# Kernel tuning notes

Measured on AMD Instinct MI355X. Metric: run time of the kernel, lower is better.

Reference implementation:

```python
import jax, jax.numpy as jnp
import numpy as np

T, WQ, WS, C, H, W = 2, 75, 25, 640, 10, 10
WAY, SHOT = 5, 5
HID = C // 16
SCALE_VALUE = 30.0
ATTEN_SCALE_VALUE = 50.0
FROM_VALUE = 0.5
VALUE_INTERVAL = 0.3
BN_EPS = 1e-5
NORM_EPS = 1e-12


def _leaky(x):
    return jnp.where(x >= 0, x, 0.2 * x)


def _l2norm(x, axis):
    n = jnp.sqrt(jnp.sum(x * x, axis=axis, keepdims=True))
    return x / jnp.maximum(n, NORM_EPS)


def _embed(x, W_conv, bn_gamma, bn_beta, bn_mean, bn_var):
    # 1x1 conv (no bias) + eval-mode BatchNorm + LeakyReLU(0.2)
    # x: [t, n, c, h, w] -> [t, n, c, h, w]
    y = jnp.einsum('oc,tnchw->tnohw', W_conv, x)
    inv = bn_gamma / jnp.sqrt(bn_var + BN_EPS)
    y = y * inv[:, None, None] + (bn_beta - bn_mean * inv)[:, None, None]
    return _leaky(y)


def setup_inputs() -> dict:
    key = jax.random.key(0)
    ks = jax.random.split(key, 5)
    return {
        'query_feat': jax.random.normal(ks[0], (T, WQ, C, H, W), dtype=jnp.float32),
        'support_feat': jax.random.normal(ks[1], (T, WS, C, H, W), dtype=jnp.float32),
        'W_conv': jax.random.normal(ks[2], (C, C), dtype=jnp.float32) * 0.02,
        'bn_gamma': jnp.ones((C,), jnp.float32),
        'bn_beta': jnp.zeros((C,), jnp.float32),
        'bn_mean': jnp.zeros((C,), jnp.float32),
        'bn_var': jnp.ones((C,), jnp.float32),
        'psi_w1': jax.random.normal(ks[3], (C, HID), dtype=jnp.float32) * 0.04,
        'psi_b1': jnp.zeros((HID,), jnp.float32),
        'psi_w2': jax.random.normal(ks[4], (HID, 1), dtype=jnp.float32) * 0.15,
        'psi_b2': jnp.zeros((1,), jnp.float32),
        'way_num': WAY,
        'shot_num': SHOT,
    }


def reference(query_feat, support_feat, W_conv, bn_gamma, bn_beta, bn_mean, bn_var,
              psi_w1, psi_b1, psi_w2, psi_b2, way_num, shot_num):
    t, wq, c, h, w = query_feat.shape
    ws = support_feat.shape[1]
    hw = h * w

    # embedded + normalized features for the gated branch
    w_query = _embed(query_feat, W_conv, bn_gamma, bn_beta, bn_mean, bn_var)
    w_query = w_query.reshape(t, wq, c, hw).transpose(0, 1, 3, 2)      # [t, wq, hw, c]
    w_support = _embed(support_feat, W_conv, bn_gamma, bn_beta, bn_mean, bn_var)
    w_support = w_support.reshape(t, ws, c, hw).transpose(0, 2, 1, 3).reshape(t, c, ws * hw)
    w_query = _l2norm(w_query, axis=3)
    w_support = _l2norm(w_support, axis=1)

    # cosine similarity of embedded features: [t, wq, hw, ws*hw]
    f_x = jnp.einsum('tqpc,tck->tqpk', w_query, w_support)

    # AEAModule: per-location adaptive threshold from f_psi MLP
    hid = _leaky(w_query @ psi_w1 + psi_b1)                            # [t, wq, hw, HID]
    clamp_value = jax.nn.sigmoid(hid @ psi_w2 + psi_b2) * VALUE_INTERVAL + FROM_VALUE
    clamp_fx = jax.nn.sigmoid(ATTEN_SCALE_VALUE * (f_x - clamp_value))
    atten_score = clamp_fx / jnp.maximum(
        jnp.sum(jnp.abs(clamp_fx), axis=-1, keepdims=True), NORM_EPS)  # L1 normalize

    # raw-feature cosine similarity
    qf = _l2norm(query_feat.reshape(t, wq, c, hw).transpose(0, 1, 3, 2), axis=3)
    sf = _l2norm(support_feat.reshape(t, ws, c, hw).transpose(0, 2, 1, 3).reshape(t, c, ws * hw), axis=1)
    match_score = jnp.einsum('tqpc,tck->tqpk', qf, sf)                 # [t, wq, hw, ws*hw]

    # gate, regroup support axis into (way, shot, hw_s), reduce
    ams = (atten_score * match_score).reshape(t, wq, hw, way_num, shot_num, hw)
    score = ams.sum(axis=-1).mean(axis=(2, 4)) * SCALE_VALUE           # [t, wq, way]
    return score
```

## Files before the change

### kernel.cpp

```cpp
#include <hip/hip_runtime.h>
#include <stdint.h>

#define T_    2
#define WQ_   75
#define WS_   25
#define C_    640
#define HW_   100
#define HID_  40
#define WAY_  5
#define QP_   (WQ_*HW_)
#define SP_   (WS_*HW_)
#define QPAD_ 128
#define KPAD_ 512
#define KROWS_ (WAY_*KPAD_)
#define C8_   (C_/8)
#define BM_   256
#define QSTR_ (C8_*QPAD_*8)

typedef _Float16 f16;
typedef _Float16 f16x8 __attribute__((ext_vector_type(8)));
typedef _Float16 f16x4 __attribute__((ext_vector_type(4)));
typedef _Float16 f16x16 __attribute__((ext_vector_type(16)));
typedef float    f32x4 __attribute__((ext_vector_type(4)));
typedef float    f32x16 __attribute__((ext_vector_type(16)));
typedef uint32_t u32;

__device__ __forceinline__ void gl_lds16(const f16* g, f16* l) {
  __builtin_amdgcn_global_load_lds(
      (const __attribute__((address_space(1))) u32*)g,
      (__attribute__((address_space(3))) u32*)l, 16, 0, 0);
}

__global__ __launch_bounds__(512) void k0_invnorm(
    const float* __restrict__ q, const float* __restrict__ s,
    float* __restrict__ rq_inv, float* __restrict__ rq_nrm,
    float* __restrict__ rs_inv, float* __restrict__ rs_nrm) {
  __shared__ float part[4][128];
  int b = blockIdx.x;
  int t = b / (WQ_ + WS_);
  int n = b % (WQ_ + WS_);
  int tid = threadIdx.x;
  int seg = tid >> 7, p = tid & 127;
  const float* base; float* oi; float* on; int idx;
  if (n < WQ_) {
    base = q + ((size_t)(t*WQ_ + n))*C_*HW_;
    idx = t*QP_ + n*HW_ + p; oi = rq_inv; on = rq_nrm;
  } else {
    int m = n - WQ_;
    base = s + ((size_t)(t*WS_ + m))*C_*HW_;
    idx = t*SP_ + m*HW_ + p; oi = rs_inv; on = rs_nrm;
  }
  float ss = 0.f;
  if (p < HW_) {
    for (int c = seg*160; c < seg*160 + 160; ++c) {
      float v = base[c*HW_ + p]; ss += v*v;
    }
  }
  part[seg][p] = ss;
  __syncthreads();
  if (seg == 0 && p < HW_) {
    float tot = part[0][p] + part[1][p] + part[2][p] + part[3][p];
    float nrm = fmaxf(sqrtf(tot), 1e-12f);
    oi[idx] = 1.f/nrm; on[idx] = nrm;
  }
}

__global__ __launch_bounds__(256) void kw_packW(
    const float* __restrict__ W, const float* __restrict__ w1,
    f16* __restrict__ Wr, f16* __restrict__ Wt8, f16* __restrict__ w1t) {
  int idx = blockIdx.x*256 + threadIdx.x;
  if (idx < C_*C8_) {
    int o = idx / C8_, c8 = idx % C8_;
    f16x8 v;
#pragma unroll
    for (int i = 0; i < 8; ++i) v[i] = (f16)W[(size_t)o*C_ + c8*8 + i];
    *reinterpret_cast<f16x8*>(Wr + (size_t)o*C_ + c8*8) = v;
    *reinterpret_cast<f16x8*>(Wt8 + ((size_t)c8*C_ + o)*8) = v;
  } else if (idx < C_*C8_ + 48*C8_) {
    int k2 = idx - C_*C8_;
    int h = k2 / C8_, c8 = k2 % C8_;
    f16x8 v;
#pragma unroll
    for (int i = 0; i < 8; ++i)
      v[i] = (h < HID_) ? (f16)w1[(size_t)(c8*8+i)*HID_ + h] : (f16)0.f;
    *reinterpret_cast<f16x8*>(w1t + (size_t)h*C_ + c8*8) = v;
  }
}

__global__ __launch_bounds__(256) void k1_pack_qraw(
    const float* __restrict__ q, const float* __restrict__ rq_inv,
    f16* __restrict__ Bq_raw) {
  int b = blockIdx.x;
  int ct = b % 10; b /= 10;
  int qq = b % WQ_; int t = b / WQ_;
  int c0 = ct*64;
  size_t tq = (size_t)t*WQ_ + qq;
  __shared__ float lds[64*HW_];
  const float4* s4 = reinterpret_cast<const float4*>(
      q + ((tq)*C_ + c0)*HW_);
  float4* l4 = reinterpret_cast<float4*>(lds);
  for (int i = threadIdx.x; i < 64*HW_/4; i += 256) l4[i] = s4[i];
  __syncthreads();
  for (int ch = threadIdx.x; ch < 8*QPAD_; ch += 256) {
    int lc8 = ch / QPAD_, p = ch % QPAD_;
    float inv = (p < HW_) ? rq_inv[t*QP_ + qq*HW_ + p] : 0.f;
    f16x8 v;
#pragma unroll
    for (int i = 0; i < 8; ++i) {
      float x = (p < HW_) ? lds[(lc8*8 + i)*HW_ + p] : 0.f;
      v[i] = (f16)(x * inv);
    }
    *reinterpret_cast<f16x8*>(Bq_raw + (tq*C8_ + c0/8 + lc8)*((size_t)QPAD_*8) + (size_t)p*8) = v;
  }
}

__global__ __launch_bounds__(256) void k2_pack_sraw(
    const float* __restrict__ s, const float* __restrict__ rs_inv,
    f16* __restrict__ As_raw) {
  int b = blockIdx.x;
  int ct = b % 10; b /= 10;
  int n = b % WS_; int t = b / WS_;
  int c0 = ct*64;
  __shared__ float lds[64*HW_];
  const float4* s4 = reinterpret_cast<const float4*>(
      s + (((size_t)(t*WS_ + n))*C_ + c0)*HW_);
  float4* l4 = reinterpret_cast<float4*>(lds);
  for (int i = threadIdx.x; i < 64*HW_/4; i += 256) l4[i] = s4[i];
  __syncthreads();
  for (int ch = threadIdx.x; ch < HW_*8; ch += 256) {
    int p = ch / 8, cc = ch % 8;
    float inv = rs_inv[t*SP_ + n*HW_ + p];
    f16x8 v;
#pragma unroll
    for (int i = 0; i < 8; ++i) v[i] = (f16)(lds[(cc*8 + i)*HW_ + p] * inv);
    int k = n*HW_ + p;
    int way = k / 500, ki = k % 500;
    size_t row = (size_t)way*KPAD_ + ki;
    *reinterpret_cast<f16x8*>(As_raw + ((size_t)(t*C8_ + c0/8 + cc)*KROWS_ + row)*8) = v;
  }
}

__global__ __launch_bounds__(512) void k3_embed_support(
    const f16* __restrict__ As_raw, const f16* __restrict__ Wt8,
    const float* __restrict__ rs_nrm,
    const float* __restrict__ g, const float* __restrict__ be,
    const float* __restrict__ mu, const float* __restrict__ va,
    f16* __restrict__ As_emb) {
  int b = blockIdx.x;
  int t = b / (KROWS_/64);
  int row0 = (b % (KROWS_/64)) * 64;
  int tid = threadIdx.x, wv = tid >> 6, lane = tid & 63;
  int mf = wv & 3, nh = wv >> 2;
  __shared__ f16 Alds[64*32];
  __shared__ f16 Blds[32*C_];
  __shared__ float rowss[64];
  f32x4 acc[20];
#pragma unroll
  for (int i = 0; i < 20; ++i) acc[i] = (f32x4){0.f,0.f,0.f,0.f};

  for (int cs = 0; cs < 20; ++cs) {
    if (tid < 256) {
      int c8l = tid >> 6, r = tid & 63;
      *reinterpret_cast<f16x8*>(Alds + (c8l*64 + r)*8) =
        *reinterpret_cast<const f16x8*>(
            As_raw + ((size_t)(t*C8_ + cs*4 + c8l)*KROWS_ + row0 + r)*8);
    }
    const f16x8* bsrc = reinterpret_cast<const f16x8*>(Wt8 + (size_t)(cs*4)*C_*8);
    f16x8* bdst = reinterpret_cast<f16x8*>(Blds);
    for (int i = tid; i < 4*C_; i += 512) bdst[i] = bsrc[i];
    __syncthreads();
    f16x8 a = *reinterpret_cast<const f16x8*>(
        Alds + ((lane>>4)*64 + mf*16 + (lane&15))*8);
#pragma unroll
    for (int nf = 0; nf < 20; ++nf) {
      int o = nh*320 + nf*16 + (lane & 15);
      f16x8 bf = *reinterpret_cast<const f16x8*>(Blds + (((lane>>4)*C_) + o)*8);
      acc[nf] = __builtin_amdgcn_mfma_f32_16x16x32_f16(a, bf, acc[nf], 0, 0, 0);
    }
    __syncthreads();
  }

  if (tid < 64) rowss[tid] = 0.f;
  __syncthreads();
  int rg = lane >> 4, cl = lane & 15;
  int prow = row0 + mf*16 + rg*4;
#pragma unroll
  for (int j = 0; j < 4; ++j) {
    int pr = prow + j;
    int way = pr / KPAD_, ki = pr - way*KPAD_;
    bool valid = ki < 500;
    float nrm = valid ? rs_nrm[t*SP_ + way*500 + ki] : 0.f;
    float ssum = 0.f;
#pragma unroll
    for (int nf = 0; nf < 20; ++nf) {
      int o = nh*320 + nf*16 + cl;
      float inv = g[o] / sqrtf(va[o] + 1e-5f);
      float sh = be[o] - mu[o]*inv;
      float y = acc[nf][j]*nrm*inv + sh;
      y = (y >= 0.f) ? y : 0.2f*y;
      if (!valid) y = 0.f;
      acc[nf][j] = y;
      ssum += y*y;
    }
#pragma unroll
    for (int m = 1; m < 16; m <<= 1) ssum += __shfl_xor(ssum, m);
    if (cl == 0) atomicAdd(&rowss[mf*16 + rg*4 + j], ssum);
  }
  __syncthreads();
#pragma unroll
  for (int j = 0; j < 4; ++j) {
    int pr = prow + j;
    int ki = pr - (pr / KPAD_)*KPAD_;
    if (ki >= 500) continue;
    float invn = 1.f / fmaxf(sqrtf(rowss[mf*16 + rg*4 + j]), 1e-12f);
#pragma unroll
    for (int nf = 0; nf < 20; ++nf) {
      int o = nh*320 + nf*16 + cl;
      As_emb[((size_t)(t*C8_ + (o>>3))*KROWS_ + pr)*8 + (o&7)] = (f16)(acc[nf][j]*invn);
    }
  }
}

__global__ __launch_bounds__(256, 3) void k4_embed_query(
    const f16* __restrict__ Wr, const f16* __restrict__ Bq_raw,
    const float* __restrict__ rq_nrm,
    const float* __restrict__ g, const float* __restrict__ be,
    const float* __restrict__ mu, const float* __restrict__ va,
    f16* __restrict__ Bq_emb) {
  __shared__ f16 Ab[3][128*32];
  __shared__ f16 Bb[3][4*QPAD_*8];
  int b = blockIdx.x;
  int ot = b % 5; b /= 5;
  int qq = b % WQ_; int t = b / WQ_;
  int o0 = ot*128;
  size_t tq = (size_t)t*WQ_ + qq;
  int tid = threadIdx.x, w = tid >> 6, lane = tid & 63;
  int la_r = lane >> 2, la_c = lane & 3;

  auto stage = [&](int buf, int cs) {
#pragma unroll
    for (int i = 0; i < 2; ++i) {
      int ca = w*2 + i;
      int r = ca*16 + la_r;
      int sc = la_c ^ (r & 3);
      gl_lds16(Wr + (size_t)(o0 + r)*C_ + cs*32 + sc*8, &Ab[buf][ca*512]);
    }
#pragma unroll
    for (int i = 0; i < 2; ++i) {
      int cb = w*2 + i;
      int c8l = cb >> 1;
      size_t src = (tq*C8_ + cs*4 + c8l)*(size_t)(QPAD_*8) + (size_t)((cb&1)*64 + lane)*8;
      gl_lds16(Bq_raw + src, &Bb[buf][(c8l*QPAD_ + (cb&1)*64)*8]);
    }
  };

  f32x4 acc[2][8];
#pragma unroll
  for (int a = 0; a < 2; ++a)
#pragma unroll
    for (int n = 0; n < 8; ++n) acc[a][n] = (f32x4){0.f,0.f,0.f,0.f};

  stage(0, 0);
  stage(1, 1);
  for (int cs = 0; cs < 20; ++cs) {
    int buf = cs % 3;
    if (cs < 19) asm volatile("s_waitcnt vmcnt(4)" ::: "memory");
    else         asm volatile("s_waitcnt vmcnt(0)" ::: "memory");
    __builtin_amdgcn_s_barrier();
    if (cs < 18) stage((cs+2)%3, cs+2);
    __builtin_amdgcn_s_setprio(1);
    f16x8 fa[2];
#pragma unroll
    for (int mi = 0; mi < 2; ++mi) {
      int R = w*32 + mi*16 + (lane & 15);
      int sc = (lane >> 4) ^ (R & 3);
      fa[mi] = *reinterpret_cast<const f16x8*>(&Ab[buf][R*32 + sc*8]);
    }
#pragma unroll
    for (int nf = 0; nf < 8; ++nf) {
      f16x8 fb = *reinterpret_cast<const f16x8*>(
          &Bb[buf][((lane>>4)*QPAD_ + nf*16 + (lane&15))*8]);
#pragma unroll
      for (int mi = 0; mi < 2; ++mi)
        acc[mi][nf] = __builtin_amdgcn_mfma_f32_16x16x32_f16(fa[mi], fb, acc[mi][nf], 0, 0, 0);
    }
    __builtin_amdgcn_s_setprio(0);
  }

#pragma unroll
  for (int mi = 0; mi < 2; ++mi) {
    int obase = o0 + w*32 + mi*16 + (lane>>4)*4;
    float inv4[4], sh4[4];
#pragma unroll
    for (int j = 0; j < 4; ++j) {
      int o = obase + j;
      inv4[j] = g[o] / sqrtf(va[o] + 1e-5f);
      sh4[j] = be[o] - mu[o]*inv4[j];
    }
#pragma unroll
    for (int nf = 0; nf < 8; ++nf) {
      int pp = nf*16 + (lane & 15);
      float nrmv = (pp < HW_) ? rq_nrm[t*QP_ + qq*HW_ + pp] : 0.f;
      f16x4 vv;
#pragma unroll
      for (int j = 0; j < 4; ++j) {
        float y = (pp < HW_) ? (acc[mi][nf][j]*nrmv*inv4[j] + sh4[j]) : 0.f;
        y = (y >= 0.f) ? y : 0.2f*y;
        vv[j] = (f16)y;
      }
      *reinterpret_cast<f16x4*>(
          &Bq_emb[(tq*C8_ + (obase>>3))*((size_t)QPAD_*8) + (size_t)pp*8 + (obase&7)]) = vv;
    }
  }
}

__global__ __launch_bounds__(256) void k5_colnorm_psi(
    const f16* __restrict__ Bq_emb, const f16* __restrict__ w1t,
    const float* __restrict__ b1, const float* __restrict__ w2,
    const float* __restrict__ b2, float* __restrict__ cv,
    float* __restrict__ invq) {
  __shared__ float ssA[2][QPAD_];
  __shared__ float invs[QPAD_];
  __shared__ float hidL[48*QPAD_];
  int bq = blockIdx.x;
  int tid = threadIdx.x, w = tid >> 6, lane = tid & 63;
  size_t base = (size_t)bq * QSTR_;

  {
    int h2 = tid >> 7, pp = tid & 127;
    float ss = 0.f;
    for (int c8 = h2*40; c8 < h2*40 + 40; ++c8) {
      f16x8 v = *reinterpret_cast<const f16x8*>(&Bq_emb[base + ((size_t)c8*QPAD_ + pp)*8]);
#pragma unroll
      for (int i = 0; i < 8; ++i) { float x = (float)v[i]; ss += x*x; }
    }
    ssA[h2][pp] = ss;
  }
  for (int i = tid; i < 48*QPAD_; i += 256) hidL[i] = 0.f;
  __syncthreads();
  if (tid < QPAD_) {
    float ss = ssA[0][tid] + ssA[1][tid];
    float inv = (ss > 0.f) ? (1.f / fmaxf(sqrtf(ss), 1e-12f)) : 0.f;
    invs[tid] = inv;
    invq[bq*QPAD_ + tid] = inv;
  }

  f32x4 acc[3][8];
#pragma unroll
  for (int a = 0; a < 3; ++a)
#pragma unroll
    for (int n = 0; n < 8; ++n) acc[a][n] = (f32x4){0.f,0.f,0.f,0.f};
  for (int r = 0; r < 5; ++r) {
    int cs = w + r*4;
    f16x8 fa[3];
#pragma unroll
    for (int mf = 0; mf < 3; ++mf) {
      int R = mf*16 + (lane & 15);
      fa[mf] = *reinterpret_cast<const f16x8*>(&w1t[(size_t)R*C_ + cs*32 + (lane>>4)*8]);
    }
#pragma unroll
    for (int nf = 0; nf < 8; ++nf) {
      f16x8 fb = *reinterpret_cast<const f16x8*>(
          &Bq_emb[base + ((size_t)(cs*4 + (lane>>4))*QPAD_ + nf*16 + (lane&15))*8]);
#pragma unroll
      for (int mf = 0; mf < 3; ++mf)
        acc[mf][nf] = __builtin_amdgcn_mfma_f32_16x16x32_f16(fa[mf], fb, acc[mf][nf], 0, 0, 0);
    }
  }
  __syncthreads();
  for (int rr = 0; rr < 4; ++rr) {
    if (w == rr) {
#pragma unroll
      for (int mf = 0; mf < 3; ++mf)
#pragma unroll
        for (int nf = 0; nf < 8; ++nf)
#pragma unroll
          for (int j = 0; j < 4; ++j) {
            int row = mf*16 + (lane>>4)*4 + j;
            int col = nf*16 + (lane & 15);
            hidL[row*QPAD_ + col] += acc[mf][nf][j];
          }
    }
    __syncthreads();
  }
  if (tid < QPAD_) {
    float inv = invs[tid];
    float z = b2[0];
    for (int h = 0; h < HID_; ++h) {
      float hv = hidL[h*QPAD_ + tid]*inv + b1[h];
      hv = (hv >= 0.f) ? hv : 0.2f*hv;
      z += hv*w2[h];
    }
    cv[bq*QPAD_ + tid] = 0.3f/(1.f + __expf(-z)) + 0.5f;
  }
}

__global__ __launch_bounds__(256, 2) void k6_main(
    const f16* __restrict__ As_emb, const f16* __restrict__ As_raw,
    const f16* __restrict__ Bq_emb, const f16* __restrict__ Bq_raw,
    const float* __restrict__ cv, const float* __restrict__ invq,
    float* __restrict__ Spart, float* __restrict__ L1part) {
  __shared__ f16 Ab[3][4*BM_*8];
  __shared__ f16 Bb[3][4*QPAD_*8];
  __shared__ float cvs[QPAD_], iqs[QPAD_], Ss[QPAD_], L1s[QPAD_];

  int bid = blockIdx.x;
  int xcd = bid & 7, j0 = bid >> 3;
  int l = (xcd < 4) ? xcd*188 + j0 : 752 + (xcd-4)*187 + j0;
  int kt = l & 1; int m = l >> 1;
  int q = m % WQ_; int gidx = m / WQ_;
  int t = gidx / WAY_, way = gidx - t*WAY_;

  int tid = threadIdx.x, w = tid >> 6, lane = tid & 63;
  size_t tq = (size_t)t*WQ_ + q;
  if (tid < QPAD_) {
    cvs[tid] = cv[tq*QPAD_ + tid];
    iqs[tid] = invq[tq*QPAD_ + tid];
    Ss[tid] = 0.f; L1s[tid] = 0.f;
  }
  int wrow0 = w*64;
  size_t rowb = (size_t)way*KPAD_ + (size_t)kt*BM_;

  const size_t aoff = ((size_t)(t*C8_ + w)*KROWS_ + rowb + lane)*8;
  const size_t boff = ((tq*C8_ + w)*(size_t)QPAD_ + lane)*8;
  const f16* pA = As_raw + aoff;
  const f16* pB = Bq_raw + boff;
  const f16* pA1 = As_emb + aoff;
  const f16* pB1 = Bq_emb + boff;
  const int CS_A = 4*KROWS_*8;
  const int CS_B = 4*QPAD_*8;

  auto stage = [&](int buf, const f16* a, const f16* bsrc) {
    f16* da = &Ab[buf][(size_t)w*BM_*8];
    f16* db = &Bb[buf][(size_t)w*QPAD_*8];
    gl_lds16(a,        da);
    gl_lds16(a + 512,  da + 512);
    gl_lds16(a + 1024, da + 1024);
    gl_lds16(a + 1536, da + 1536);
    gl_lds16(bsrc,       db);
    gl_lds16(bsrc + 512, db + 512);
  };

  f32x16 acc[2][4];
  f16x16 mtc[2][4];
#pragma unroll
  for (int mi = 0; mi < 2; ++mi)
#pragma unroll
    for (int nf = 0; nf < 4; ++nf) acc[mi][nf] = (f32x16)(0.f);
  float Sl[4] = {0,0,0,0}, L1l[4] = {0,0,0,0};

  stage(0, pA, pB); pA += CS_A; pB += CS_B;
  stage(1, pA, pB); pA += CS_A; pB += CS_B;

  for (int ph = 0; ph < 40; ++ph) {
    if (ph == 18) { pA = pA1; pB = pB1; }
    int buf = ph % 3;
    if (ph < 39) asm volatile("s_waitcnt vmcnt(6)" ::: "memory");
    else         asm volatile("s_waitcnt vmcnt(0)" ::: "memory");
    __builtin_amdgcn_s_barrier();
    if (ph < 38) { stage((ph+2)%3, pA, pB); pA += CS_A; pB += CS_B; }
    __builtin_amdgcn_s_setprio(1);
    const f16* Abuf = Ab[buf];
    const f16* Bbuf = Bb[buf];
    int r0 = wrow0 + (lane & 31);
#pragma unroll
    for (int ks = 0; ks < 2; ++ks) {
      int c8l = ks*2 + (lane >> 5);
      f16x8 fa0 = *reinterpret_cast<const f16x8*>(&Abuf[(c8l*BM_ + r0)*8]);
      f16x8 fa1 = *reinterpret_cast<const f16x8*>(&Abuf[(c8l*BM_ + r0 + 32)*8]);
#pragma unroll
      for (int nf = 0; nf < 4; ++nf) {
        f16x8 fb = *reinterpret_cast<const f16x8*>(
            &Bbuf[(c8l*QPAD_ + nf*32 + (lane & 31))*8]);
        acc[0][nf] = __builtin_amdgcn_mfma_f32_32x32x16_f16(fa0, fb, acc[0][nf], 0, 0, 0);
        acc[1][nf] = __builtin_amdgcn_mfma_f32_32x32x16_f16(fa1, fb, acc[1][nf], 0, 0, 0);
      }
    }
    __builtin_amdgcn_s_setprio(0);

    if (ph == 19) {
#pragma unroll
      for (int mi = 0; mi < 2; ++mi)
#pragma unroll
        for (int nf = 0; nf < 4; ++nf) {
#pragma unroll
          for (int jj = 0; jj < 16; ++jj) {
            mtc[mi][nf][jj] = (f16)fminf(fmaxf(acc[mi][nf][jj], -8.f), 8.f);
            acc[mi][nf][jj] = 0.f;
          }
        }
    } else if (ph == 39) {
#pragma unroll
      for (int nf = 0; nf < 4; ++nf) {
        int col = nf*32 + (lane & 31);
        float cvv = cvs[col];
        float iq = iqs[col];
#pragma unroll
        for (int mi = 0; mi < 2; ++mi)
#pragma unroll
          for (int jj = 0; jj < 16; ++jj) {
            float fx = acc[mi][nf][jj] * iq;
            float sg = 1.f/(1.f + __expf(-50.f*(fx - cvv)));
            Sl[nf]  += sg * (float)mtc[mi][nf][jj];
            L1l[nf] += sg;
          }
      }
    }
  }

#pragma unroll
  for (int nf = 0; nf < 4; ++nf) {
    float vs = Sl[nf] + __shfl_xor(Sl[nf], 32);
    float vl = L1l[nf] + __shfl_xor(L1l[nf], 32);
    if (lane < 32) {
      atomicAdd(&Ss[nf*32 + lane], vs);
      atomicAdd(&L1s[nf*32 + lane], vl);
    }
  }
  __syncthreads();
  if (tid < QPAD_) {
    size_t o = ((tq*WAY_ + way)*2 + kt)*(size_t)QPAD_ + tid;
    Spart[o] = Ss[tid]; L1part[o] = L1s[tid];
  }
}

__global__ __launch_bounds__(128) void k7_reduce(
    const float* __restrict__ Spart, const float* __restrict__ L1part,
    float* __restrict__ out) {
  int b = blockIdx.x;
  int tid = threadIdx.x;
  __shared__ float red[128];
  float contrib[WAY_] = {0,0,0,0,0};
  if (tid < HW_) {
    size_t base = (size_t)b*WAY_*2*QPAD_;
    float l1 = 0.f;
#pragma unroll
    for (int w = 0; w < WAY_; ++w)
#pragma unroll
      for (int k = 0; k < 2; ++k) l1 += L1part[base + (w*2+k)*QPAD_ + tid];
    l1 = fmaxf(l1, 1e-12f);
#pragma unroll
    for (int w = 0; w < WAY_; ++w)
      contrib[w] = (Spart[base + (w*2+0)*QPAD_ + tid] +
                    Spart[base + (w*2+1)*QPAD_ + tid]) / l1;
  }
#pragma unroll
  for (int w = 0; w < WAY_; ++w) {
    red[tid] = contrib[w];
    __syncthreads();
    for (int off = 64; off > 0; off >>= 1) {
      if (tid < off) red[tid] += red[tid + off];
      __syncthreads();
    }
    if (tid == 0) out[b*WAY_ + w] = red[0] * 30.f / (float)(HW_*5);
    __syncthreads();
  }
}

extern "C" void kernel_launch(void* const* d_in, const int* in_sizes, int n_in,
                              void* d_out, int out_size, void* d_ws, size_t ws_size,
                              hipStream_t stream) {
  (void)in_sizes; (void)n_in; (void)out_size; (void)ws_size;
  const float* q  = (const float*)d_in[0];
  const float* s  = (const float*)d_in[1];
  const float* W  = (const float*)d_in[2];
  const float* g  = (const float*)d_in[3];
  const float* be = (const float*)d_in[4];
  const float* mu = (const float*)d_in[5];
  const float* va = (const float*)d_in[6];
  const float* w1 = (const float*)d_in[7];
  const float* b1 = (const float*)d_in[8];
  const float* w2 = (const float*)d_in[9];
  const float* b2 = (const float*)d_in[10];
  float* out = (float*)d_out;
  char* ws = (char*)d_ws;

  size_t off = 0;
  auto nxt = [&](size_t bytes) { size_t o = off; off += (bytes + 255) & ~(size_t)255; return o; };
  float* rq_inv = (float*)(ws + nxt((size_t)T_*QP_*4));
  float* rq_nrm = (float*)(ws + nxt((size_t)T_*QP_*4));
  float* rs_inv = (float*)(ws + nxt((size_t)T_*SP_*4));
  float* rs_nrm = (float*)(ws + nxt((size_t)T_*SP_*4));
  f16* Wr     = (f16*)(ws + nxt((size_t)C_*C_*2));
  f16* Wt8    = (f16*)(ws + nxt((size_t)C_*C_*2));
  f16* w1t    = (f16*)(ws + nxt((size_t)48*C_*2));
  f16* As_raw = (f16*)(ws + nxt((size_t)T_*KROWS_*C_*2));
  f16* As_emb = (f16*)(ws + nxt((size_t)T_*KROWS_*C_*2));
  f16* Bq_raw = (f16*)(ws + nxt((size_t)T_*WQ_*QSTR_*2));
  f16* Bq_emb = (f16*)(ws + nxt((size_t)T_*WQ_*QSTR_*2));
  float* cvp    = (float*)(ws + nxt((size_t)T_*WQ_*QPAD_*4));
  float* invq   = (float*)(ws + nxt((size_t)T_*WQ_*QPAD_*4));
  float* Spart  = (float*)(ws + nxt((size_t)T_*WQ_*WAY_*2*QPAD_*4));
  float* L1part = (float*)(ws + nxt((size_t)T_*WQ_*WAY_*2*QPAD_*4));

  hipMemsetAsync(As_raw, 0, (size_t)T_*KROWS_*C_*2, stream);
  hipMemsetAsync(As_emb, 0, (size_t)T_*KROWS_*C_*2, stream);

  k0_invnorm<<<T_*(WQ_+WS_), 512, 0, stream>>>(q, s, rq_inv, rq_nrm, rs_inv, rs_nrm);
  kw_packW<<<(C_*C8_ + 48*C8_ + 255)/256, 256, 0, stream>>>(W, w1, Wr, Wt8, w1t);
  k1_pack_qraw<<<T_*WQ_*10, 256, 0, stream>>>(q, rq_inv, Bq_raw);
  k2_pack_sraw<<<T_*WS_*10, 256, 0, stream>>>(s, rs_inv, As_raw);
  k3_embed_support<<<T_*(KROWS_/64), 512, 0, stream>>>(As_raw, Wt8, rs_nrm, g, be, mu, va, As_emb);
  k4_embed_query<<<T_*WQ_*5, 256, 0, stream>>>(Wr, Bq_raw, rq_nrm, g, be, mu, va, Bq_emb);
  k5_colnorm_psi<<<T_*WQ_, 256, 0, stream>>>(Bq_emb, w1t, b1, w2, b2, cvp, invq);
  k6_main<<<1500, 256, 0, stream>>>(As_emb, As_raw, Bq_emb, Bq_raw, cvp, invq, Spart, L1part);
  k7_reduce<<<T_*WQ_, 128, 0, stream>>>(Spart, L1part, out);
}
```

Before: 311.6 us.

## Halve tile heights in support-embed and main kernels to double block count

The main similarity kernel now uses 128-row support tiles instead of 256, so it launches 3000 blocks with a 4-way split per (query, way). Each wave holds a single 32x32 accumulator row set, which is meant to cut registers and LDS enough for 3 blocks per CU. The XCD remapping, staging loads and reduction are adjusted to match. The support embedding kernel likewise moves to 32-row tiles for more blocks. In exchange, each block does less work per load of the query B tile, which is now reloaded more often, and partial sums double.

```diff
diff --git a/kernel.cpp b/kernel.cpp
--- a/kernel.cpp
+++ b/kernel.cpp
@@ -14,7 +14,7 @@
 #define KPAD_ 512
 #define KROWS_ (WAY_*KPAD_)
 #define C8_   (C_/8)
-#define BM_   256
+#define BM_   128
 #define QSTR_ (C8_*QPAD_*8)
 
 typedef _Float16 f16;
@@ -147,21 +147,21 @@
     const float* __restrict__ mu, const float* __restrict__ va,
     f16* __restrict__ As_emb) {
   int b = blockIdx.x;
-  int t = b / (KROWS_/64);
-  int row0 = (b % (KROWS_/64)) * 64;
+  int t = b / (KROWS_/32);
+  int row0 = (b % (KROWS_/32)) * 32;
   int tid = threadIdx.x, wv = tid >> 6, lane = tid & 63;
-  int mf = wv & 3, nh = wv >> 2;
-  __shared__ f16 Alds[64*32];
+  int mf = wv & 1, nh = wv >> 1;
+  __shared__ f16 Alds[32*32];
   __shared__ f16 Blds[32*C_];
-  __shared__ float rowss[64];
-  f32x4 acc[20];
-#pragma unroll
-  for (int i = 0; i < 20; ++i) acc[i] = (f32x4){0.f,0.f,0.f,0.f};
+  __shared__ float rowss[32];
+  f32x4 acc[10];
+#pragma unroll
+  for (int i = 0; i < 10; ++i) acc[i] = (f32x4){0.f,0.f,0.f,0.f};
 
   for (int cs = 0; cs < 20; ++cs) {
-    if (tid < 256) {
-      int c8l = tid >> 6, r = tid & 63;
-      *reinterpret_cast<f16x8*>(Alds + (c8l*64 + r)*8) =
+    if (tid < 128) {
+      int c8l = tid >> 5, r = tid & 31;
+      *reinterpret_cast<f16x8*>(Alds + (c8l*32 + r)*8) =
         *reinterpret_cast<const f16x8*>(
             As_raw + ((size_t)(t*C8_ + cs*4 + c8l)*KROWS_ + row0 + r)*8);
     }
@@ -170,20 +170,21 @@
     for (int i = tid; i < 4*C_; i += 512) bdst[i] = bsrc[i];
     __syncthreads();
     f16x8 a = *reinterpret_cast<const f16x8*>(
-        Alds + ((lane>>4)*64 + mf*16 + (lane&15))*8);
-#pragma unroll
-    for (int nf = 0; nf < 20; ++nf) {
-      int o = nh*320 + nf*16 + (lane & 15);
+        Alds + ((lane>>4)*32 + mf*16 + (lane&15))*8);
+#pragma unroll
+    for (int nf = 0; nf < 10; ++nf) {
+      int o = nh*160 + nf*16 + (lane & 15);
       f16x8 bf = *reinterpret_cast<const f16x8*>(Blds + (((lane>>4)*C_) + o)*8);
       acc[nf] = __builtin_amdgcn_mfma_f32_16x16x32_f16(a, bf, acc[nf], 0, 0, 0);
     }
     __syncthreads();
   }
 
-  if (tid < 64) rowss[tid] = 0.f;
+  if (tid < 32) rowss[tid] = 0.f;
   __syncthreads();
   int rg = lane >> 4, cl = lane & 15;
-  int prow = row0 + mf*16 + rg*4;
+  int lrow = mf*16 + rg*4;
+  int prow = row0 + lrow;
 #pragma unroll
   for (int j = 0; j < 4; ++j) {
     int pr = prow + j;
@@ -192,8 +193,8 @@
     float nrm = valid ? rs_nrm[t*SP_ + way*500 + ki] : 0.f;
     float ssum = 0.f;
 #pragma unroll
-    for (int nf = 0; nf < 20; ++nf) {
-      int o = nh*320 + nf*16 + cl;
+    for (int nf = 0; nf < 10; ++nf) {
+      int o = nh*160 + nf*16 + cl;
       float inv = g[o] / sqrtf(va[o] + 1e-5f);
       float sh = be[o] - mu[o]*inv;
       float y = acc[nf][j]*nrm*inv + sh;
@@ -204,7 +205,7 @@
     }
 #pragma unroll
     for (int m = 1; m < 16; m <<= 1) ssum += __shfl_xor(ssum, m);
-    if (cl == 0) atomicAdd(&rowss[mf*16 + rg*4 + j], ssum);
+    if (cl == 0) atomicAdd(&rowss[lrow + j], ssum);
   }
   __syncthreads();
 #pragma unroll
@@ -212,10 +213,10 @@
     int pr = prow + j;
     int ki = pr - (pr / KPAD_)*KPAD_;
     if (ki >= 500) continue;
-    float invn = 1.f / fmaxf(sqrtf(rowss[mf*16 + rg*4 + j]), 1e-12f);
-#pragma unroll
-    for (int nf = 0; nf < 20; ++nf) {
-      int o = nh*320 + nf*16 + cl;
+    float invn = 1.f / fmaxf(sqrtf(rowss[lrow + j]), 1e-12f);
+#pragma unroll
+    for (int nf = 0; nf < 10; ++nf) {
+      int o = nh*160 + nf*16 + cl;
       As_emb[((size_t)(t*C8_ + (o>>3))*KROWS_ + pr)*8 + (o&7)] = (f16)(acc[nf][j]*invn);
     }
   }
@@ -395,7 +396,7 @@
   }
 }
 
-__global__ __launch_bounds__(256, 2) void k6_main(
+__global__ __launch_bounds__(256, 3) void k6_main(
     const f16* __restrict__ As_emb, const f16* __restrict__ As_raw,
     const f16* __restrict__ Bq_emb, const f16* __restrict__ Bq_raw,
     const float* __restrict__ cv, const float* __restrict__ invq,
@@ -405,9 +406,8 @@
   __shared__ float cvs[QPAD_], iqs[QPAD_], Ss[QPAD_], L1s[QPAD_];
 
   int bid = blockIdx.x;
-  int xcd = bid & 7, j0 = bid >> 3;
-  int l = (xcd < 4) ? xcd*188 + j0 : 752 + (xcd-4)*187 + j0;
-  int kt = l & 1; int m = l >> 1;
+  int l = (bid & 7)*375 + (bid >> 3);
+  int kt = l & 3; int m = l >> 2;
   int q = m % WQ_; int gidx = m / WQ_;
   int t = gidx / WAY_, way = gidx - t*WAY_;
 
@@ -418,35 +418,31 @@
     iqs[tid] = invq[tq*QPAD_ + tid];
     Ss[tid] = 0.f; L1s[tid] = 0.f;
   }
-  int wrow0 = w*64;
+  int wrow0 = w*32;
   size_t rowb = (size_t)way*KPAD_ + (size_t)kt*BM_;
 
-  const size_t aoff = ((size_t)(t*C8_ + w)*KROWS_ + rowb + lane)*8;
-  const size_t boff = ((tq*C8_ + w)*(size_t)QPAD_ + lane)*8;
+  const size_t aoff = ((size_t)(t*C8_ + (w>>1))*KROWS_ + rowb + (w&1)*64 + lane)*8;
+  const size_t boff = ((tq*C8_ + (w>>1))*(size_t)QPAD_ + (w&1)*64 + lane)*8;
   const f16* pA = As_raw + aoff;
   const f16* pB = Bq_raw + boff;
   const f16* pA1 = As_emb + aoff;
   const f16* pB1 = Bq_emb + boff;
   const int CS_A = 4*KROWS_*8;
   const int CS_B = 4*QPAD_*8;
+  const int A2 = 2*KROWS_*8;
+  const int B2 = 2*QPAD_*8;
 
   auto stage = [&](int buf, const f16* a, const f16* bsrc) {
-    f16* da = &Ab[buf][(size_t)w*BM_*8];
-    f16* db = &Bb[buf][(size_t)w*QPAD_*8];
-    gl_lds16(a,        da);
-    gl_lds16(a + 512,  da + 512);
-    gl_lds16(a + 1024, da + 1024);
-    gl_lds16(a + 1536, da + 1536);
-    gl_lds16(bsrc,       db);
-    gl_lds16(bsrc + 512, db + 512);
+    gl_lds16(a,      &Ab[buf][w*512]);
+    gl_lds16(a + A2, &Ab[buf][(w+4)*512]);
+    gl_lds16(bsrc,      &Bb[buf][w*512]);
+    gl_lds16(bsrc + B2, &Bb[buf][(w+4)*512]);
   };
 
-  f32x16 acc[2][4];
-  f16x16 mtc[2][4];
-#pragma unroll
-  for (int mi = 0; mi < 2; ++mi)
-#pragma unroll
-    for (int nf = 0; nf < 4; ++nf) acc[mi][nf] = (f32x16)(0.f);
+  f32x16 acc[4];
+  f16x16 mtc[4];
+#pragma unroll
+  for (int nf = 0; nf < 4; ++nf) acc[nf] = (f32x16)(0.f);
   float Sl[4] = {0,0,0,0}, L1l[4] = {0,0,0,0};
 
   stage(0, pA, pB); pA += CS_A; pB += CS_B;
@@ -455,7 +451,7 @@
   for (int ph = 0; ph < 40; ++ph) {
     if (ph == 18) { pA = pA1; pB = pB1; }
     int buf = ph % 3;
-    if (ph < 39) asm volatile("s_waitcnt vmcnt(6)" ::: "memory");
+    if (ph < 39) asm volatile("s_waitcnt vmcnt(4)" ::: "memory");
     else         asm volatile("s_waitcnt vmcnt(0)" ::: "memory");
     __builtin_amdgcn_s_barrier();
     if (ph < 38) { stage((ph+2)%3, pA, pB); pA += CS_A; pB += CS_B; }
@@ -466,28 +462,23 @@
 #pragma unroll
     for (int ks = 0; ks < 2; ++ks) {
       int c8l = ks*2 + (lane >> 5);
-      f16x8 fa0 = *reinterpret_cast<const f16x8*>(&Abuf[(c8l*BM_ + r0)*8]);
-      f16x8 fa1 = *reinterpret_cast<const f16x8*>(&Abuf[(c8l*BM_ + r0 + 32)*8]);
+      f16x8 fa = *reinterpret_cast<const f16x8*>(&Abuf[(c8l*BM_ + r0)*8]);
 #pragma unroll
       for (int nf = 0; nf < 4; ++nf) {
         f16x8 fb = *reinterpret_cast<const f16x8*>(
             &Bbuf[(c8l*QPAD_ + nf*32 + (lane & 31))*8]);
-        acc[0][nf] = __builtin_amdgcn_mfma_f32_32x32x16_f16(fa0, fb, acc[0][nf], 0, 0, 0);
-        acc[1][nf] = __builtin_amdgcn_mfma_f32_32x32x16_f16(fa1, fb, acc[1][nf], 0, 0, 0);
+        acc[nf] = __builtin_amdgcn_mfma_f32_32x32x16_f16(fa, fb, acc[nf], 0, 0, 0);
       }
     }
     __builtin_amdgcn_s_setprio(0);
 
     if (ph == 19) {
 #pragma unroll
-      for (int mi = 0; mi < 2; ++mi)
-#pragma unroll
-        for (int nf = 0; nf < 4; ++nf) {
-#pragma unroll
-          for (int jj = 0; jj < 16; ++jj) {
-            mtc[mi][nf][jj] = (f16)fminf(fmaxf(acc[mi][nf][jj], -8.f), 8.f);
-            acc[mi][nf][jj] = 0.f;
-          }
+      for (int nf = 0; nf < 4; ++nf)
+#pragma unroll
+        for (int jj = 0; jj < 16; ++jj) {
+          mtc[nf][jj] = (f16)fminf(fmaxf(acc[nf][jj], -8.f), 8.f);
+          acc[nf][jj] = 0.f;
         }
     } else if (ph == 39) {
 #pragma unroll
@@ -496,14 +487,12 @@
         float cvv = cvs[col];
         float iq = iqs[col];
 #pragma unroll
-        for (int mi = 0; mi < 2; ++mi)
-#pragma unroll
-          for (int jj = 0; jj < 16; ++jj) {
-            float fx = acc[mi][nf][jj] * iq;
-            float sg = 1.f/(1.f + __expf(-50.f*(fx - cvv)));
-            Sl[nf]  += sg * (float)mtc[mi][nf][jj];
-            L1l[nf] += sg;
-          }
+        for (int jj = 0; jj < 16; ++jj) {
+          float fx = acc[nf][jj] * iq;
+          float sg = 1.f/(1.f + __expf(-50.f*(fx - cvv)));
+          Sl[nf]  += sg * (float)mtc[nf][jj];
+          L1l[nf] += sg;
+        }
       }
     }
   }
@@ -519,7 +508,7 @@
   }
   __syncthreads();
   if (tid < QPAD_) {
-    size_t o = ((tq*WAY_ + way)*2 + kt)*(size_t)QPAD_ + tid;
+    size_t o = ((tq*WAY_ + way)*4 + kt)*(size_t)QPAD_ + tid;
     Spart[o] = Ss[tid]; L1part[o] = L1s[tid];
   }
 }
@@ -532,17 +521,20 @@
   __shared__ float red[128];
   float contrib[WAY_] = {0,0,0,0,0};
   if (tid < HW_) {
-    size_t base = (size_t)b*WAY_*2*QPAD_;
+    size_t base = (size_t)b*WAY_*4*QPAD_;
     float l1 = 0.f;
 #pragma unroll
     for (int w = 0; w < WAY_; ++w)
 #pragma unroll
-      for (int k = 0; k < 2; ++k) l1 += L1part[base + (w*2+k)*QPAD_ + tid];
+      for (int k = 0; k < 4; ++k) l1 += L1part[base + (w*4+k)*QPAD_ + tid];
     l1 = fmaxf(l1, 1e-12f);
 #pragma unroll
-    for (int w = 0; w < WAY_; ++w)
-      contrib[w] = (Spart[base + (w*2+0)*QPAD_ + tid] +
-                    Spart[base + (w*2+1)*QPAD_ + tid]) / l1;
+    for (int w = 0; w < WAY_; ++w) {
+      float sv = 0.f;
+#pragma unroll
+      for (int k = 0; k < 4; ++k) sv += Spart[base + (w*4+k)*QPAD_ + tid];
+      contrib[w] = sv / l1;
+    }
   }
 #pragma unroll
   for (int w = 0; w < WAY_; ++w) {
@@ -590,8 +582,8 @@
   f16* Bq_emb = (f16*)(ws + nxt((size_t)T_*WQ_*QSTR_*2));
   float* cvp    = (float*)(ws + nxt((size_t)T_*WQ_*QPAD_*4));
   float* invq   = (float*)(ws + nxt((size_t)T_*WQ_*QPAD_*4));
-  float* Spart  = (float*)(ws + nxt((size_t)T_*WQ_*WAY_*2*QPAD_*4));
-  float* L1part = (float*)(ws + nxt((size_t)T_*WQ_*WAY_*2*QPAD_*4));
+  float* Spart  = (float*)(ws + nxt((size_t)T_*WQ_*WAY_*4*QPAD_*4));
+  float* L1part = (float*)(ws + nxt((size_t)T_*WQ_*WAY_*4*QPAD_*4));
 
   hipMemsetAsync(As_raw, 0, (size_t)T_*KROWS_*C_*2, stream);
   hipMemsetAsync(As_emb, 0, (size_t)T_*KROWS_*C_*2, stream);
@@ -600,9 +592,9 @@
   kw_packW<<<(C_*C8_ + 48*C8_ + 255)/256, 256, 0, stream>>>(W, w1, Wr, Wt8, w1t);
   k1_pack_qraw<<<T_*WQ_*10, 256, 0, stream>>>(q, rq_inv, Bq_raw);
   k2_pack_sraw<<<T_*WS_*10, 256, 0, stream>>>(s, rs_inv, As_raw);
-  k3_embed_support<<<T_*(KROWS_/64), 512, 0, stream>>>(As_raw, Wt8, rs_nrm, g, be, mu, va, As_emb);
+  k3_embed_support<<<T_*(KROWS_/32), 512, 0, stream>>>(As_raw, Wt8, rs_nrm, g, be, mu, va, As_emb);
   k4_embed_query<<<T_*WQ_*5, 256, 0, stream>>>(Wr, Bq_raw, rq_nrm, g, be, mu, va, Bq_emb);
   k5_colnorm_psi<<<T_*WQ_, 256, 0, stream>>>(Bq_emb, w1t, b1, w2, b2, cvp, invq);
-  k6_main<<<1500, 256, 0, stream>>>(As_emb, As_raw, Bq_emb, Bq_raw, cvp, invq, Spart, L1part);
+  k6_main<<<3000, 256, 0, stream>>>(As_emb, As_raw, Bq_emb, Bq_raw, cvp, invq, Spart, L1part);
   k7_reduce<<<T_*WQ_, 128, 0, stream>>>(Spart, L1part, out);
 }
```

Result: no change. 312.2 us (+0.2%).
